# Kernel tuning notes

Hardware: AMD Instinct MI355X
Metric: run time of the kernel (lower is better)

The kernel has to match this reference:

```python
import jax, jax.numpy as jnp
import numpy as np

N = 100_000      # nodes
E = 1_600_000    # edges (avg degree 16)
FIN = 128
FOUT = 64
C = 1.0          # Poincare ball curvature (args.c)
T = 0.48         # threshold (forward default)
MIN_NORM = 1e-15
PROJ_EPS = 4e-3  # float32 boundary eps used by standard PoincareBall.proj


def _artanh(x):
    x = jnp.clip(x, -1.0 + 1e-7, 1.0 - 1e-7)
    return 0.5 * (jnp.log1p(x) - jnp.log1p(-x))


def logmap0(p, c):
    sc = c ** 0.5
    n = jnp.clip(jnp.linalg.norm(p, axis=-1, keepdims=True), MIN_NORM, None)
    return p / (sc * n) * _artanh(sc * n)


def expmap0(u, c):
    sc = c ** 0.5
    n = jnp.clip(jnp.linalg.norm(u, axis=-1, keepdims=True), MIN_NORM, None)
    return jnp.tanh(sc * n) * u / (sc * n)


def proj(x, c):
    n = jnp.clip(jnp.linalg.norm(x, axis=-1, keepdims=True), MIN_NORM, None)
    maxn = (1.0 - PROJ_EPS) / (c ** 0.5)
    return jnp.where(n > maxn, x / n * maxn, x)


def setup_inputs() -> dict:
    key = jax.random.key(0)
    k0, k1, k2, k3, k4 = jax.random.split(key, 5)
    # points near the origin of the Poincare ball
    x = jax.random.normal(k0, (N, FIN), dtype=jnp.float32) * 0.05
    edge_index = jax.random.randint(k1, (2, E), 0, N, dtype=jnp.int32)
    W_up = jax.random.normal(k2, (FIN, FOUT), dtype=jnp.float32) / np.float32(np.sqrt(FIN))
    W_pl = jax.random.normal(k3, (FOUT, 2), dtype=jnp.float32) / np.float32(np.sqrt(FOUT))
    W_lw = jax.random.normal(k4, (2 * FOUT, 1), dtype=jnp.float32) / np.float32(np.sqrt(2 * FOUT))
    return {"x": x, "edge_index": edge_index, "W_up": W_up, "W_pl": W_pl, "W_lw": W_lw}


def reference(x, edge_index, W_up, W_pl, W_lw):
    src, dst = edge_index[0], edge_index[1]

    def agg(v):  # PyG add-aggregation: out[i] = sum_{(j->i)} v[j]
        return jax.ops.segment_sum(v[src], dst, num_segments=N)

    x_tan = logmap0(x, C)                                   # [N, FIN]
    updated_x = jax.nn.leaky_relu(x_tan @ W_up)             # [N, FOUT], slope 0.01
    sum_neigh = agg(updated_x)                              # [N, FOUT]
    random_prob = jax.nn.softmax(jax.nn.relu(sum_neigh @ W_pl), axis=-1)  # [N, 2]
    sel_v = jnp.where(random_prob[:, 1:2] > T, 1.0, 0.0)    # [N, 1] hard gate
    sum_sel = agg(sel_v * updated_x)                        # [N, FOUT]
    weight_sel = jax.nn.sigmoid(jnp.concatenate([sum_sel, sum_neigh], axis=-1) @ W_lw)  # [N, 1]
    a_x = jax.nn.relu(agg(weight_sel * sel_v * updated_x))  # [N, FOUT]
    out = updated_x + a_x
    return proj(expmap0(out, C), C)
```

## Files before the change

### kernel.cpp

```cpp
#include <hip/hip_runtime.h>
#include <math.h>

#define FIN 128
#define FOUT 64
#define MAXDEG 64
#define BKT_SHIFT 7
#define BKT_CAP 2560


__device__ __forceinline__ float4 f4add(float4 a, float4 b) {
  return make_float4(a.x + b.x, a.y + b.y, a.z + b.z, a.w + b.w);
}
__device__ __forceinline__ float4 f4fma(float c, float4 v, float4 a) {
  return make_float4(fmaf(c, v.x, a.x), fmaf(c, v.y, a.y),
                     fmaf(c, v.z, a.z), fmaf(c, v.w, a.w));
}
__device__ __forceinline__ float red16(float v) {
  v += __shfl_xor(v, 1, 64);
  v += __shfl_xor(v, 2, 64);
  v += __shfl_xor(v, 4, 64);
  v += __shfl_xor(v, 8, 64);
  return v;
}

__device__ __forceinline__ float row_scale(float ss) {
  float n  = sqrtf(ss);
  float nc = fmaxf(n, 1e-15f);
  float t  = fminf(nc, 1.0f - 1e-7f);
  float at = 0.5f * (log1pf(t) - log1pf(-t));
  return at / nc;
}

__device__ __forceinline__ float leaky(float v) {
  return (v >= 0.f) ? v : 0.01f * v;
}

__device__ __forceinline__ unsigned int bf16rne(float x) {
  unsigned int b = __float_as_uint(x);
  b += 0x7FFFu + ((b >> 16) & 1u);
  return b >> 16;
}
__device__ __forceinline__ float4 bf4(uint2 v) {
  return make_float4(__uint_as_float(v.x << 16),
                     __uint_as_float(v.x & 0xFFFF0000u),
                     __uint_as_float(v.y << 16),
                     __uint_as_float(v.y & 0xFFFF0000u));
}

__global__ __launch_bounds__(256) void k_main(const float* __restrict__ x,
                                              const float* __restrict__ Wup,
                                              const float* __restrict__ Wpl,
                                              const float* __restrict__ Wlw,
                                              float* __restrict__ u,
                                              float* __restrict__ scl4,
                                              const int* __restrict__ ei, int E,
                                              int nb, int* __restrict__ bcnt,
                                              int2* __restrict__ stg,
                                              int N, int gemmBlocks) {
  __shared__ float buf[8192];
  __shared__ float wls[256];
  __shared__ float ps[256];
  __shared__ float scl[64];

  int t = threadIdx.x;

  if (blockIdx.x >= gemmBlocks) {
    int* hist = (int*)buf;
    int* base = hist + nb;
    int bb = blockIdx.x - gemmBlocks;
    for (int h = t; h < nb; h += 256) hist[h] = 0;
    __syncthreads();
    int e0 = bb * 4096 + t * 16;
    int sv[16], dv[16];
#pragma unroll
    for (int j = 0; j < 16; j += 4) {
      int e = e0 + j;
      if (e + 3 < E) {
        int4 s4 = *(const int4*)(ei + e);
        int4 d4 = *(const int4*)(ei + E + e);
        sv[j] = s4.x; sv[j+1] = s4.y; sv[j+2] = s4.z; sv[j+3] = s4.w;
        dv[j] = d4.x; dv[j+1] = d4.y; dv[j+2] = d4.z; dv[j+3] = d4.w;
      } else {
        for (int q = 0; q < 4; ++q) {
          int ee = e + q;
          sv[j+q] = (ee < E) ? ei[ee] : -1;
          dv[j+q] = (ee < E) ? ei[E + ee] : -1;
        }
      }
    }
#pragma unroll
    for (int j = 0; j < 16; ++j)
      if (dv[j] >= 0) atomicAdd(&hist[dv[j] >> BKT_SHIFT], 1);
    __syncthreads();
    for (int h = t; h < nb; h += 256)
      base[h] = hist[h] ? atomicAdd(&bcnt[h], hist[h]) : 0;
    __syncthreads();
    for (int h = t; h < nb; h += 256) hist[h] = 0;
    __syncthreads();
#pragma unroll
    for (int j = 0; j < 16; ++j) {
      if (dv[j] < 0) continue;
      int b = dv[j] >> BKT_SHIFT;
      int p = base[b] + atomicAdd(&hist[b], 1);
      if (p < BKT_CAP) stg[(size_t)b * BKT_CAP + p] = make_int2(sv[j], dv[j]);
    }
    return;
  }

  int n0 = blockIdx.x * 64;
  {
    int proj = t >> 6, f = t & 63;
    float wv = (proj == 0) ? Wpl[f * 2]
             : (proj == 1) ? Wpl[f * 2 + 1]
             : (proj == 2) ? Wlw[f] : Wlw[64 + f];
    wls[t] = wv;
  }

  {
    int n  = t & 63;
    int kq = t >> 6;
    int gn = n0 + n;
    bool ok = gn < N;
    const float4* xr = (const float4*)(x + (size_t)gn * FIN);
    float ssum = 0.f;
    float4 r0[8];
#pragma unroll
    for (int m = 0; m < 8; ++m)
      r0[m] = ok ? xr[kq * 8 + m] : make_float4(0.f, 0.f, 0.f, 0.f);
#pragma unroll
    for (int m = 0; m < 8; ++m) {
      float4 v = r0[m];
      ssum = fmaf(v.x, v.x, fmaf(v.y, v.y, fmaf(v.z, v.z, fmaf(v.w, v.w, ssum))));
      int kf = kq * 32 + m * 4;
      buf[(kf + 0) * 64 + n] = v.x;
      buf[(kf + 1) * 64 + n] = v.y;
      buf[(kf + 2) * 64 + n] = v.z;
      buf[(kf + 3) * 64 + n] = v.w;
    }
    ps[t] = ssum;
  }
  __syncthreads();
  if (t < 64) scl[t] = row_scale(ps[t] + ps[t + 64] + ps[t + 128] + ps[t + 192]);

  int wave = t >> 6, lane = t & 63;
  int j = lane & 3, i = lane >> 2;
  const float* xp = buf + i * 4;
  const float* wg = Wup + wave * 16 + j * 4;
  float4 a0 = make_float4(0,0,0,0), a1 = a0, a2 = a0, a3 = a0;
#pragma unroll 8
  for (int k = 0; k < FIN; ++k) {
    float4 xv = *(const float4*)(xp + k * 64);
    float4 wv = *(const float4*)(wg + k * 64);
    a0 = f4fma(xv.x, wv, a0);
    a1 = f4fma(xv.y, wv, a1);
    a2 = f4fma(xv.z, wv, a2);
    a3 = f4fma(xv.w, wv, a3);
  }
  __syncthreads();

  int fbase = wave * 16 + j * 4;
#pragma unroll
  for (int r = 0; r < 4; ++r) {
    float4 acc = (r == 0) ? a0 : (r == 1) ? a1 : (r == 2) ? a2 : a3;
    int nn = i * 4 + r;
    int gnn = n0 + nn;
    float sc = scl[nn];
    float4 o = make_float4(leaky(sc * acc.x), leaky(sc * acc.y),
                           leaky(sc * acc.z), leaky(sc * acc.w));
    if (gnn < N) *(float4*)(u + (size_t)gnn * FOUT + fbase) = o;
    buf[nn * 67 + fbase]     = o.x;
    buf[nn * 67 + fbase + 1] = o.y;
    buf[nn * 67 + fbase + 2] = o.z;
    buf[nn * 67 + fbase + 3] = o.w;
  }
  __syncthreads();

  {
    int proj = t >> 6;
    const float* wc = wls + proj * 64;
    int nn = t & 63;
    int gnn = n0 + nn;
    const float* ur = buf + nn * 67;
    float acc = 0.f;
#pragma unroll 8
    for (int f = 0; f < 64; ++f) acc = fmaf(ur[f], wc[f], acc);
    if (gnn < N) scl4[(size_t)gnn * 4 + proj] = acc;
  }
}

__global__ __launch_bounds__(256) void k_place(const int2* __restrict__ stg,
                                               const int* __restrict__ bcnt,
                                               const float4* __restrict__ scl4,
                                               int* __restrict__ deg,
                                               int* __restrict__ slots,
                                               float2* __restrict__ gs,
                                               float* __restrict__ tp, int N) {
  __shared__ int slds[128 * MAXDEG];
  __shared__ int cur[128];
  int b = blockIdx.x, t = threadIdx.x;
  if (t < 128) cur[t] = 0;
  __syncthreads();
  int cnt = min(bcnt[b], BKT_CAP);
  int dbase = b << BKT_SHIFT;
  const int2* sp = stg + (size_t)b * BKT_CAP;
  for (int i = t; i < cnt; i += 256) {
    int2 e = sp[i];
    int dl = e.y - dbase;
    int p = atomicAdd(&cur[dl], 1);
    if (p < MAXDEG) slds[dl * MAXDEG + p] = e.x;
  }
  __syncthreads();

  int nrows = min(128, N - dbase);
  if (t < 128 && t < nrows) deg[dbase + t] = min(cur[t], MAXDEG);

  {
    int4* gdst = (int4*)(slots + (size_t)dbase * MAXDEG);
    const int4* lsrc = (const int4*)slds;
#pragma unroll
    for (int q = 0; q < 8; ++q) {
      int jj = q * 256 + t;
      if ((jj >> 4) < nrows) gdst[jj] = lsrc[jj];
    }
  }

  int grp = t >> 4, l16 = t & 15;
#pragma unroll
  for (int rep = 0; rep < 8; ++rep) {
    int nl = rep * 16 + grp;
    int i  = dbase + nl;
    bool act = (i < N);
    int d = act ? min(cur[nl], MAXDEG) : 0;
    float ax = 0.f, ay = 0.f, aw = 0.f;
#pragma unroll
    for (int q = 0; q < 4; ++q) {
      int k = l16 + q * 16;
      if (k < d) {
        int s = slds[nl * MAXDEG + k];
        float4 gg = scl4[s];
        ax += gg.x; ay += gg.y; aw += gg.w;
      }
    }
    ax = red16(ax); ay = red16(ay); aw = red16(aw);
    if (act && l16 == 0) {
      float r0 = fmaxf(ax, 0.f), r1 = fmaxf(ay, 0.f);
      float m  = fmaxf(r0, r1);
      float e0 = expf(r0 - m), e1 = expf(r1 - m);
      float p  = e1 / (e0 + e1);
      float sel = (p > 0.48f) ? 1.f : 0.f;
      float4 own = scl4[i];
      gs[i] = make_float2(sel, sel * own.z);
      tp[i] = aw;
    }
  }
}

__global__ __launch_bounds__(256) void k_wgt(const int* __restrict__ deg,
                                             int* __restrict__ slots,
                                             const float2* __restrict__ gs,
                                             const float* __restrict__ tp,
                                             const float* __restrict__ u,
                                             unsigned int* __restrict__ uw,
                                             int* __restrict__ scnt, int N) {
  if (blockIdx.x == 0 && threadIdx.x < 32)
    uw[(size_t)N * 32 + threadIdx.x] = 0u;
  int wv = threadIdx.x >> 6, lane = threadIdx.x & 63;
  int g = lane >> 4, l16 = lane & 15;
  int i = blockIdx.x * 16 + wv * 4 + g;
  bool act = (i < N);
  int d = act ? deg[i] : 0;
  int sv[4]; bool f[4];
  float a = 0.f;
#pragma unroll
  for (int q = 0; q < 4; ++q) {
    int k = l16 + q * 16;
    bool valid = k < d;
    int s = 0;
    if (valid) s = slots[(size_t)i * MAXDEG + k];
    sv[q] = s;
    float2 gv = make_float2(0.f, 0.f);
    if (valid) gv = gs[s];
    f[q] = valid && (gv.x != 0.f);
    a += gv.y;
  }
  a = red16(a);
  unsigned long long m0 = __ballot(f[0]);
  unsigned long long m1 = __ballot(f[1]);
  unsigned long long m2 = __ballot(f[2]);
  unsigned long long m3 = __ballot(f[3]);
  int sh = g * 16;
  unsigned gm0 = (unsigned)(m0 >> sh) & 0xFFFFu;
  unsigned gm1 = (unsigned)(m1 >> sh) & 0xFFFFu;
  unsigned gm2 = (unsigned)(m2 >> sh) & 0xFFFFu;
  unsigned gm3 = (unsigned)(m3 >> sh) & 0xFFFFu;
  int c0 = __popc(gm0), c1 = __popc(gm1), c2 = __popc(gm2);
  unsigned lm = (1u << l16) - 1u;
  int r0 = __popc(gm0 & lm);
  int r1 = c0 + __popc(gm1 & lm);
  int r2 = c0 + c1 + __popc(gm2 & lm);
  int r3 = c0 + c1 + c2 + __popc(gm3 & lm);
  if (!act) return;
  if (f[0]) slots[(size_t)i * MAXDEG + r0] = sv[0];
  if (f[1]) slots[(size_t)i * MAXDEG + r1] = sv[1];
  if (f[2]) slots[(size_t)i * MAXDEG + r2] = sv[2];
  if (f[3]) slots[(size_t)i * MAXDEG + r3] = sv[3];
  if (l16 == 0) scnt[i] = c0 + c1 + c2 + __popc(gm3);
  if (gs[i].x != 0.f) {
    float sig = 1.f / (1.f + expf(-(tp[i] + a)));
    float4 uv = ((const float4*)(u + (size_t)i * 64))[l16];
    unsigned int b0 = bf16rne(sig * uv.x), b1 = bf16rne(sig * uv.y);
    unsigned int b2 = bf16rne(sig * uv.z), b3 = bf16rne(sig * uv.w);
    ((uint2*)(uw + (size_t)i * 32))[l16] =
        make_uint2(b0 | (b1 << 16), b2 | (b3 << 16));
  }
}

__global__ __launch_bounds__(256) void k_agg3(const int* __restrict__ scnt,
                                              const int* __restrict__ slots,
                                              const uint2* __restrict__ uw,
                                              const float* __restrict__ u,
                                              float* __restrict__ out, int N) {
  __shared__ int comp[16][64];
  int wv = threadIdx.x >> 6, lane = threadIdx.x & 63;
  int g = lane >> 4, l16 = lane & 15;
  int nloc = wv * 4 + g;
  int i = blockIdx.x * 16 + nloc;
  bool act = (i < N);
  int sc = act ? scnt[i] : 0;
#pragma unroll
  for (int b = 0; b < 4; ++b) {
    int idx = b * 16 + l16;
    comp[nloc][idx] = (idx < sc) ? slots[(size_t)i * MAXDEG + idx] : N;
  }
  float4 acc = make_float4(0.f, 0.f, 0.f, 0.f);
  for (int r = 0; r < sc; r += 4) {
#pragma unroll
    for (int j = 0; j < 4; ++j) {
      int s = (r + j < sc) ? comp[nloc][r + j] : N;
      uint2 w = uw[(size_t)s * 16 + l16];
      acc = f4add(acc, bf4(w));
    }
  }
  if (!act) return;
  float4 uv = ((const float4*)(u + (size_t)i * 64))[l16];
  float4 ov = make_float4(uv.x + fmaxf(acc.x, 0.f), uv.y + fmaxf(acc.y, 0.f),
                          uv.z + fmaxf(acc.z, 0.f), uv.w + fmaxf(acc.w, 0.f));
  float ssp = ov.x * ov.x + ov.y * ov.y + ov.z * ov.z + ov.w * ov.w;
  float ss  = red16(ssp);
  float nc  = fmaxf(sqrtf(ss), 1e-15f);
  float th  = tanhf(nc);
  float fac = th / nc;
  float4 r = make_float4(ov.x * fac, ov.y * fac, ov.z * fac, ov.w * fac);
  float n2 = fmaxf(th, 1e-15f);
  float maxn = 1.0f - 4e-3f;
  float sc2 = (n2 > maxn) ? (maxn / n2) : 1.0f;
  float4 res = make_float4(r.x * sc2, r.y * sc2, r.z * sc2, r.w * sc2);
  ((float4*)(out + (size_t)i * 64))[l16] = res;
}

extern "C" void kernel_launch(void* const* d_in, const int* in_sizes, int n_in,
                              void* d_out, int out_size, void* d_ws, size_t ws_size,
                              hipStream_t stream) {
  const float* x   = (const float*)d_in[0];
  const int*   ei  = (const int*)d_in[1];
  const float* Wup = (const float*)d_in[2];
  const float* Wpl = (const float*)d_in[3];
  const float* Wlw = (const float*)d_in[4];
  float* out = (float*)d_out;

  int N = in_sizes[0] / FIN;
  int E = in_sizes[1] / 2;
  int nb = (N + (1 << BKT_SHIFT) - 1) >> BKT_SHIFT;

  char* ws = (char*)d_ws;
  float* u     = (float*)ws;
  int*   slots = (int*)(u + (size_t)N * 64);
  char*  regB  = (char*)(slots + (size_t)N * MAXDEG);
  size_t regB_sz = (size_t)nb * BKT_CAP * sizeof(int2);
  int2*  stg   = (int2*)regB;
  unsigned int* uwp = (unsigned int*)regB;
  float* scl4  = (float*)(regB + regB_sz);
  int*   deg   = (int*)(scl4 + (size_t)N * 4);
  float2* gs   = (float2*)(deg + N);
  float* tp    = (float*)(gs + N);
  int*   scnt  = (int*)(tp + N);
  int*   bcnt  = scnt + N;

  hipMemsetAsync(bcnt, 0, nb * sizeof(int), stream);

  int gemmBlocks = (N + 63) / 64;
  int binABlocks = (E + 4095) / 4096;
  k_main<<<gemmBlocks + binABlocks, 256, 0, stream>>>(
      x, Wup, Wpl, Wlw, u, scl4, ei, E, nb, bcnt, stg, N, gemmBlocks);
  k_place<<<nb, 256, 0, stream>>>(stg, bcnt, (const float4*)scl4, deg, slots, gs, tp, N);
  int nblk16 = (N + 15) / 16;
  k_wgt<<<nblk16, 256, 0, stream>>>(deg, slots, (const float2*)gs, tp, u, uwp, scnt, N);
  k_agg3<<<nblk16, 256, 0, stream>>>(scnt, slots, (const uint2*)uwp, u, out, N);
}
```

Measured before the change: 200.8 us.

## Fuse place, weight and aggregate stages into one cooperative kernel with LDS slots

Replaces the three tail kernels (place, weight, aggregate) with one cooperative kernel of one block per 128-node bucket, using grid-wide syncs between phases. Each block keeps its neighbour lists, selected counts, gates and partial logits in shared memory instead of writing and re-reading the global slots, deg, tp and scnt arrays. This removes two kernel launches and most of the adjacency-list global traffic. In exchange the gather phases run with far fewer blocks and waves per CU, which may hurt latency hiding. It also depends on the whole grid being co-resident for the cooperative launch.

Result: slower. 489.2 us (+143.6%).

```diff
diff --git a/kernel.cpp b/kernel.cpp
--- a/kernel.cpp
+++ b/kernel.cpp
@@ -1,4 +1,5 @@
 #include <hip/hip_runtime.h>
+#include <hip/hip_cooperative_groups.h>
 #include <math.h>
 
 #define FIN 128
@@ -6,6 +7,8 @@
 #define MAXDEG 64
 #define BKT_SHIFT 7
 #define BKT_CAP 2560
+
+namespace cg = cooperative_groups;
 
 
 __device__ __forceinline__ float4 f4add(float4 a, float4 b) {
@@ -188,20 +191,28 @@
   }
 }
 
-__global__ __launch_bounds__(256) void k_place(const int2* __restrict__ stg,
-                                               const int* __restrict__ bcnt,
-                                               const float4* __restrict__ scl4,
-                                               int* __restrict__ deg,
-                                               int* __restrict__ slots,
-                                               float2* __restrict__ gs,
-                                               float* __restrict__ tp, int N) {
-  __shared__ int slds[128 * MAXDEG];
-  __shared__ int cur[128];
+__global__ __launch_bounds__(256, 4) void k_tail(const int2* __restrict__ stg,
+                                                 const int* __restrict__ bcnt,
+                                                 const float4* __restrict__ scl4,
+                                                 const float* __restrict__ u,
+                                                 float2* __restrict__ gs,
+                                                 unsigned int* __restrict__ uw,
+                                                 float* __restrict__ out, int N) {
+  __shared__ int   slds[128 * MAXDEG];
+  __shared__ int   cur[128];
+  __shared__ int   scntl[128];
+  __shared__ float tps[128];
+  __shared__ float sell[128];
+  cg::grid_group grid = cg::this_grid();
+
   int b = blockIdx.x, t = threadIdx.x;
+  int dbase = b << BKT_SHIFT;
+  int grp = t >> 4, l16 = t & 15;
+  int lane = t & 63, gw = lane >> 4;
+
   if (t < 128) cur[t] = 0;
   __syncthreads();
   int cnt = min(bcnt[b], BKT_CAP);
-  int dbase = b << BKT_SHIFT;
   const int2* sp = stg + (size_t)b * BKT_CAP;
   for (int i = t; i < cnt; i += 256) {
     int2 e = sp[i];
@@ -211,20 +222,6 @@
   }
   __syncthreads();
 
-  int nrows = min(128, N - dbase);
-  if (t < 128 && t < nrows) deg[dbase + t] = min(cur[t], MAXDEG);
-
-  {
-    int4* gdst = (int4*)(slots + (size_t)dbase * MAXDEG);
-    const int4* lsrc = (const int4*)slds;
-#pragma unroll
-    for (int q = 0; q < 8; ++q) {
-      int jj = q * 256 + t;
-      if ((jj >> 4) < nrows) gdst[jj] = lsrc[jj];
-    }
-  }
-
-  int grp = t >> 4, l16 = t & 15;
 #pragma unroll
   for (int rep = 0; rep < 8; ++rep) {
     int nl = rep * 16 + grp;
@@ -250,112 +247,98 @@
       float sel = (p > 0.48f) ? 1.f : 0.f;
       float4 own = scl4[i];
       gs[i] = make_float2(sel, sel * own.z);
-      tp[i] = aw;
-    }
-  }
-}
-
-__global__ __launch_bounds__(256) void k_wgt(const int* __restrict__ deg,
-                                             int* __restrict__ slots,
-                                             const float2* __restrict__ gs,
-                                             const float* __restrict__ tp,
-                                             const float* __restrict__ u,
-                                             unsigned int* __restrict__ uw,
-                                             int* __restrict__ scnt, int N) {
-  if (blockIdx.x == 0 && threadIdx.x < 32)
-    uw[(size_t)N * 32 + threadIdx.x] = 0u;
-  int wv = threadIdx.x >> 6, lane = threadIdx.x & 63;
-  int g = lane >> 4, l16 = lane & 15;
-  int i = blockIdx.x * 16 + wv * 4 + g;
-  bool act = (i < N);
-  int d = act ? deg[i] : 0;
-  int sv[4]; bool f[4];
-  float a = 0.f;
-#pragma unroll
-  for (int q = 0; q < 4; ++q) {
-    int k = l16 + q * 16;
-    bool valid = k < d;
-    int s = 0;
-    if (valid) s = slots[(size_t)i * MAXDEG + k];
-    sv[q] = s;
-    float2 gv = make_float2(0.f, 0.f);
-    if (valid) gv = gs[s];
-    f[q] = valid && (gv.x != 0.f);
-    a += gv.y;
-  }
-  a = red16(a);
-  unsigned long long m0 = __ballot(f[0]);
-  unsigned long long m1 = __ballot(f[1]);
-  unsigned long long m2 = __ballot(f[2]);
-  unsigned long long m3 = __ballot(f[3]);
-  int sh = g * 16;
-  unsigned gm0 = (unsigned)(m0 >> sh) & 0xFFFFu;
-  unsigned gm1 = (unsigned)(m1 >> sh) & 0xFFFFu;
-  unsigned gm2 = (unsigned)(m2 >> sh) & 0xFFFFu;
-  unsigned gm3 = (unsigned)(m3 >> sh) & 0xFFFFu;
-  int c0 = __popc(gm0), c1 = __popc(gm1), c2 = __popc(gm2);
-  unsigned lm = (1u << l16) - 1u;
-  int r0 = __popc(gm0 & lm);
-  int r1 = c0 + __popc(gm1 & lm);
-  int r2 = c0 + c1 + __popc(gm2 & lm);
-  int r3 = c0 + c1 + c2 + __popc(gm3 & lm);
-  if (!act) return;
-  if (f[0]) slots[(size_t)i * MAXDEG + r0] = sv[0];
-  if (f[1]) slots[(size_t)i * MAXDEG + r1] = sv[1];
-  if (f[2]) slots[(size_t)i * MAXDEG + r2] = sv[2];
-  if (f[3]) slots[(size_t)i * MAXDEG + r3] = sv[3];
-  if (l16 == 0) scnt[i] = c0 + c1 + c2 + __popc(gm3);
-  if (gs[i].x != 0.f) {
-    float sig = 1.f / (1.f + expf(-(tp[i] + a)));
+      tps[nl]  = aw;
+      sell[nl] = sel;
+    }
+  }
+  __threadfence();
+  grid.sync();
+
+  if (b == 0 && t < 32) uw[(size_t)N * 32 + t] = 0u;
+  for (int rep = 0; rep < 8; ++rep) {
+    int nl = rep * 16 + grp;
+    int i  = dbase + nl;
+    bool act = (i < N);
+    int d = act ? min(cur[nl], MAXDEG) : 0;
+    int sv[4]; bool f[4];
+    float a = 0.f;
+#pragma unroll
+    for (int q = 0; q < 4; ++q) {
+      int k = l16 + q * 16;
+      bool valid = k < d;
+      int s = 0;
+      if (valid) s = slds[nl * MAXDEG + k];
+      sv[q] = s;
+      float2 gv = make_float2(0.f, 0.f);
+      if (valid) gv = gs[s];
+      f[q] = valid && (gv.x != 0.f);
+      a += gv.y;
+    }
+    a = red16(a);
+    unsigned long long m0 = __ballot(f[0]);
+    unsigned long long m1 = __ballot(f[1]);
+    unsigned long long m2 = __ballot(f[2]);
+    unsigned long long m3 = __ballot(f[3]);
+    int sh = gw * 16;
+    unsigned gm0 = (unsigned)(m0 >> sh) & 0xFFFFu;
+    unsigned gm1 = (unsigned)(m1 >> sh) & 0xFFFFu;
+    unsigned gm2 = (unsigned)(m2 >> sh) & 0xFFFFu;
+    unsigned gm3 = (unsigned)(m3 >> sh) & 0xFFFFu;
+    int c0 = __popc(gm0), c1 = __popc(gm1), c2 = __popc(gm2);
+    unsigned lm = (1u << l16) - 1u;
+    int r0 = __popc(gm0 & lm);
+    int r1 = c0 + __popc(gm1 & lm);
+    int r2 = c0 + c1 + __popc(gm2 & lm);
+    int r3 = c0 + c1 + c2 + __popc(gm3 & lm);
+    if (f[0]) slds[nl * MAXDEG + r0] = sv[0];
+    if (f[1]) slds[nl * MAXDEG + r1] = sv[1];
+    if (f[2]) slds[nl * MAXDEG + r2] = sv[2];
+    if (f[3]) slds[nl * MAXDEG + r3] = sv[3];
+    if (act && l16 == 0) scntl[nl] = c0 + c1 + c2 + __popc(gm3);
+    if (act && sell[nl] != 0.f) {
+      float sig = 1.f / (1.f + expf(-(tps[nl] + a)));
+      float4 uv = ((const float4*)(u + (size_t)i * 64))[l16];
+      unsigned int b0 = bf16rne(sig * uv.x), b1 = bf16rne(sig * uv.y);
+      unsigned int b2 = bf16rne(sig * uv.z), b3 = bf16rne(sig * uv.w);
+      ((uint2*)(uw + (size_t)i * 32))[l16] =
+          make_uint2(b0 | (b1 << 16), b2 | (b3 << 16));
+    }
+  }
+  __threadfence();
+  grid.sync();
+
+  const uint2* uw2 = (const uint2*)uw;
+  for (int rep = 0; rep < 8; ++rep) {
+    int nl = rep * 16 + grp;
+    int i  = dbase + nl;
+    bool act = (i < N);
+    int sc = act ? scntl[nl] : 0;
+    float4 acc = make_float4(0.f, 0.f, 0.f, 0.f);
+    for (int r = 0; r < sc; r += 4) {
+#pragma unroll
+      for (int j = 0; j < 4; ++j) {
+        int idx = r + j;
+        int s = (idx < sc) ? slds[nl * MAXDEG + idx] : N;
+        uint2 w = uw2[(size_t)s * 16 + l16];
+        acc = f4add(acc, bf4(w));
+      }
+    }
+    if (!act) continue;
     float4 uv = ((const float4*)(u + (size_t)i * 64))[l16];
-    unsigned int b0 = bf16rne(sig * uv.x), b1 = bf16rne(sig * uv.y);
-    unsigned int b2 = bf16rne(sig * uv.z), b3 = bf16rne(sig * uv.w);
-    ((uint2*)(uw + (size_t)i * 32))[l16] =
-        make_uint2(b0 | (b1 << 16), b2 | (b3 << 16));
-  }
-}
-
-__global__ __launch_bounds__(256) void k_agg3(const int* __restrict__ scnt,
-                                              const int* __restrict__ slots,
-                                              const uint2* __restrict__ uw,
-                                              const float* __restrict__ u,
-                                              float* __restrict__ out, int N) {
-  __shared__ int comp[16][64];
-  int wv = threadIdx.x >> 6, lane = threadIdx.x & 63;
-  int g = lane >> 4, l16 = lane & 15;
-  int nloc = wv * 4 + g;
-  int i = blockIdx.x * 16 + nloc;
-  bool act = (i < N);
-  int sc = act ? scnt[i] : 0;
-#pragma unroll
-  for (int b = 0; b < 4; ++b) {
-    int idx = b * 16 + l16;
-    comp[nloc][idx] = (idx < sc) ? slots[(size_t)i * MAXDEG + idx] : N;
-  }
-  float4 acc = make_float4(0.f, 0.f, 0.f, 0.f);
-  for (int r = 0; r < sc; r += 4) {
-#pragma unroll
-    for (int j = 0; j < 4; ++j) {
-      int s = (r + j < sc) ? comp[nloc][r + j] : N;
-      uint2 w = uw[(size_t)s * 16 + l16];
-      acc = f4add(acc, bf4(w));
-    }
-  }
-  if (!act) return;
-  float4 uv = ((const float4*)(u + (size_t)i * 64))[l16];
-  float4 ov = make_float4(uv.x + fmaxf(acc.x, 0.f), uv.y + fmaxf(acc.y, 0.f),
-                          uv.z + fmaxf(acc.z, 0.f), uv.w + fmaxf(acc.w, 0.f));
-  float ssp = ov.x * ov.x + ov.y * ov.y + ov.z * ov.z + ov.w * ov.w;
-  float ss  = red16(ssp);
-  float nc  = fmaxf(sqrtf(ss), 1e-15f);
-  float th  = tanhf(nc);
-  float fac = th / nc;
-  float4 r = make_float4(ov.x * fac, ov.y * fac, ov.z * fac, ov.w * fac);
-  float n2 = fmaxf(th, 1e-15f);
-  float maxn = 1.0f - 4e-3f;
-  float sc2 = (n2 > maxn) ? (maxn / n2) : 1.0f;
-  float4 res = make_float4(r.x * sc2, r.y * sc2, r.z * sc2, r.w * sc2);
-  ((float4*)(out + (size_t)i * 64))[l16] = res;
+    float4 ov = make_float4(uv.x + fmaxf(acc.x, 0.f), uv.y + fmaxf(acc.y, 0.f),
+                            uv.z + fmaxf(acc.z, 0.f), uv.w + fmaxf(acc.w, 0.f));
+    float ssp = ov.x * ov.x + ov.y * ov.y + ov.z * ov.z + ov.w * ov.w;
+    float ss  = red16(ssp);
+    float nc  = fmaxf(sqrtf(ss), 1e-15f);
+    float th  = tanhf(nc);
+    float fac = th / nc;
+    float4 r4 = make_float4(ov.x * fac, ov.y * fac, ov.z * fac, ov.w * fac);
+    float n2 = fmaxf(th, 1e-15f);
+    float maxn = 1.0f - 4e-3f;
+    float sc2 = (n2 > maxn) ? (maxn / n2) : 1.0f;
+    float4 res = make_float4(r4.x * sc2, r4.y * sc2, r4.z * sc2, r4.w * sc2);
+    ((float4*)(out + (size_t)i * 64))[l16] = res;
+  }
 }
 
 extern "C" void kernel_launch(void* const* d_in, const int* in_sizes, int n_in,
@@ -374,26 +357,27 @@
 
   char* ws = (char*)d_ws;
   float* u     = (float*)ws;
-  int*   slots = (int*)(u + (size_t)N * 64);
-  char*  regB  = (char*)(slots + (size_t)N * MAXDEG);
+  char*  regB  = (char*)(u + (size_t)N * 64);
   size_t regB_sz = (size_t)nb * BKT_CAP * sizeof(int2);
   int2*  stg   = (int2*)regB;
   unsigned int* uwp = (unsigned int*)regB;
   float* scl4  = (float*)(regB + regB_sz);
-  int*   deg   = (int*)(scl4 + (size_t)N * 4);
-  float2* gs   = (float2*)(deg + N);
-  float* tp    = (float*)(gs + N);
-  int*   scnt  = (int*)(tp + N);
-  int*   bcnt  = scnt + N;
-
-  hipMemsetAsync(bcnt, 0, nb * sizeof(int), stream);
+  float2* gs   = (float2*)(scl4 + (size_t)N * 4);
+  int*   bcnt  = (int*)(gs + N);
+
+  (void)hipMemsetAsync(bcnt, 0, nb * sizeof(int), stream);
 
   int gemmBlocks = (N + 63) / 64;
   int binABlocks = (E + 4095) / 4096;
   k_main<<<gemmBlocks + binABlocks, 256, 0, stream>>>(
       x, Wup, Wpl, Wlw, u, scl4, ei, E, nb, bcnt, stg, N, gemmBlocks);
-  k_place<<<nb, 256, 0, stream>>>(stg, bcnt, (const float4*)scl4, deg, slots, gs, tp, N);
-  int nblk16 = (N + 15) / 16;
-  k_wgt<<<nblk16, 256, 0, stream>>>(deg, slots, (const float2*)gs, tp, u, uwp, scnt, N);
-  k_agg3<<<nblk16, 256, 0, stream>>>(scnt, slots, (const uint2*)uwp, u, out, N);
-}
+
+  const int2*   stgc  = stg;
+  const int*    bcntc = bcnt;
+  const float4* scl4c = (const float4*)scl4;
+  const float*  uc    = u;
+  void* kargs[] = {(void*)&stgc, (void*)&bcntc, (void*)&scl4c, (void*)&uc,
+                   (void*)&gs, (void*)&uwp, (void*)&out, (void*)&N};
+  (void)hipLaunchCooperativeKernel((const void*)k_tail, dim3(nb), dim3(256),
+                                   kargs, 0, stream);
+}
```
